# Kernel tuning notes

Measured on AMD Instinct MI355X. Metric: run time of the kernel, lower is better.

Reference implementation:

```python
import jax, jax.numpy as jnp
import numpy as np

NUM_HEADS = 8
KEY_DIM = 256
VALUE_DIM = 256


def setup_inputs() -> dict:
    key = jax.random.key(0)
    kx, km, kq, kk, kv, ko = jax.random.split(key, 6)
    x = jax.random.normal(kx, (8, 32, 32, KEY_DIM), dtype=jnp.float32)
    m = jax.random.normal(km, (8, 32, 32, KEY_DIM), dtype=jnp.float32)
    query_proj = jax.random.normal(kq, (NUM_HEADS, KEY_DIM, KEY_DIM), dtype=jnp.float32)
    key_proj = jax.random.normal(kk, (KEY_DIM, KEY_DIM), dtype=jnp.float32)
    value_proj = jax.random.normal(kv, (KEY_DIM, VALUE_DIM), dtype=jnp.float32)
    output_proj = jax.random.normal(ko, (KEY_DIM, NUM_HEADS, VALUE_DIM), dtype=jnp.float32)
    return {"x": x, "m": m, "query_proj": query_proj, "key_proj": key_proj,
            "value_proj": value_proj, "output_proj": output_proj}


def reference(x, m, query_proj, key_proj, value_proj, output_proj):
    b = x.shape[0]
    d = x.shape[-1]  # == key_dim
    xr = x.reshape(b, -1, d)   # [b, n, d]
    mr = m.reshape(b, -1, d)   # [b, s, d]
    # Per-head query projection; shared (multi-query) key/value projections.
    q = jnp.einsum('bnd,hdk->bnhk', xr, query_proj)            # [b, n, h, k]
    k = jnp.einsum('bsd,dk->bsk', mr, key_proj)                # [b, s, k] shared across heads
    logits = jnp.einsum('bnhk,bsk->bnhs', q, k) / jnp.sqrt(jnp.asarray(d, x.dtype))
    attn = jax.nn.softmax(logits, axis=-1)                      # dropout p=0.0 -> identity
    v = jnp.einsum('bsd,dv->bsv', mr, value_proj)              # [b, s, v] shared across heads
    o = jnp.einsum('bnhs,bsv->bnhv', attn, v)                  # [b, n, h, v]
    out = jnp.einsum('bnhv,dhv->bnd', o, output_proj)          # back to key_dim channels
    return out.reshape(x.shape)
```

## Files before the change

### kernel.cpp

```cpp
#include <hip/hip_runtime.h>
#include <math.h>


typedef short bf16x8 __attribute__((ext_vector_type(8)));
typedef float f32x4  __attribute__((ext_vector_type(4)));

#define MFMA(a, b, c) __builtin_amdgcn_mfma_f32_16x16x32_bf16((a), (b), (c), 0, 0, 0)

typedef __attribute__((address_space(3))) unsigned int lds_u32_t;
typedef __attribute__((address_space(1))) const unsigned int glb_u32_t;

__device__ __forceinline__ unsigned short f32_bf16(float f) {
  unsigned u = __float_as_uint(f);
  u += 0x7FFFu + ((u >> 16) & 1u);
  return (unsigned short)(u >> 16);
}
__device__ __forceinline__ float bf16_f32(unsigned short h) {
  return __uint_as_float(((unsigned)h) << 16);
}

__global__ void k_prep(const float* __restrict__ x, const float* __restrict__ m,
                       const float* __restrict__ op, const float* __restrict__ qp,
                       const float* __restrict__ kp, const float* __restrict__ vp,
                       unsigned short* __restrict__ xh, unsigned short* __restrict__ xl,
                       unsigned short* __restrict__ mh, unsigned short* __restrict__ ml,
                       unsigned short* __restrict__ opb,
                       unsigned short* __restrict__ qph, unsigned short* __restrict__ qpl,
                       unsigned short* __restrict__ kph, unsigned short* __restrict__ kpl,
                       unsigned short* __restrict__ vpt) {
  const int tid = blockIdx.x * blockDim.x + threadIdx.x;
  const int stride = gridDim.x * blockDim.x;
  for (int i = tid; i < 2097152; i += stride) {
    float v = x[i];
    unsigned short h = f32_bf16(v);
    xh[i] = h; xl[i] = f32_bf16(v - bf16_f32(h));
    float w = m[i];
    unsigned short h2 = f32_bf16(w);
    mh[i] = h2; ml[i] = f32_bf16(w - bf16_f32(h2));
  }
  for (int i = tid; i < 524288; i += stride) {
    opb[i] = f32_bf16(op[i]);
    float q = qp[i];
    unsigned short h = f32_bf16(q);
    qph[i] = h; qpl[i] = f32_bf16(q - bf16_f32(h));
  }
  for (int i = tid; i < 65536; i += stride) {
    float k = kp[i];
    unsigned short h = f32_bf16(k);
    kph[i] = h; kpl[i] = f32_bf16(k - bf16_f32(h));
    const int vc = i >> 8, d = i & 255;
    vpt[i] = f32_bf16(vp[d * 256 + vc]);
  }
}

__global__ __launch_bounds__(256) void k_w(
    const unsigned short* __restrict__ qph, const unsigned short* __restrict__ qpl,
    const unsigned short* __restrict__ kph, const unsigned short* __restrict__ kpl,
    unsigned short* __restrict__ wh, unsigned short* __restrict__ wl) {
  const int jt = blockIdx.x & 7;
  const int h  = blockIdx.x >> 3;
  const int wave = threadIdx.x >> 6;
  const int lane = threadIdx.x & 63;
  const int lr = lane & 15, lg = lane >> 4;

  f32x4 acc[2][4];
  const f32x4 z = {0.f, 0.f, 0.f, 0.f};
#pragma unroll
  for (int mi = 0; mi < 2; ++mi)
#pragma unroll
    for (int nt = 0; nt < 4; ++nt) acc[mi][nt] = z;

  for (int ks = 0; ks < 8; ++ks) {
    bf16x8 ah[2], al[2], bh[4], bl[4];
#pragma unroll
    for (int mi = 0; mi < 2; ++mi) {
      const size_t aoff = ((size_t)(jt * 32 + mi * 16 + lr)) * 256 + ks * 32 + lg * 8;
      ah[mi] = *(const bf16x8*)(kph + aoff);
      al[mi] = *(const bf16x8*)(kpl + aoff);
    }
#pragma unroll
    for (int nt = 0; nt < 4; ++nt) {
      const size_t boff = ((size_t)(h * 256 + wave * 64 + nt * 16 + lr)) * 256 + ks * 32 + lg * 8;
      bh[nt] = *(const bf16x8*)(qph + boff);
      bl[nt] = *(const bf16x8*)(qpl + boff);
    }
#pragma unroll
    for (int nt = 0; nt < 4; ++nt)
#pragma unroll
      for (int mi = 0; mi < 2; ++mi) {
        acc[mi][nt] = MFMA(ah[mi], bh[nt], acc[mi][nt]);
        acc[mi][nt] = MFMA(ah[mi], bl[nt], acc[mi][nt]);
        acc[mi][nt] = MFMA(al[mi], bh[nt], acc[mi][nt]);
      }
  }
#pragma unroll
  for (int mi = 0; mi < 2; ++mi)
#pragma unroll
    for (int nt = 0; nt < 4; ++nt)
#pragma unroll
      for (int r = 0; r < 4; ++r) {
        const int j = jt * 32 + mi * 16 + lg * 4 + r;
        const int i = wave * 64 + nt * 16 + lr;
        const float v = acc[mi][nt][r];
        const size_t idx = ((size_t)(h * 256 + j)) * 256 + i;
        const unsigned short hi = f32_bf16(v);
        wh[idx] = hi;
        wl[idx] = f32_bf16(v - bf16_f32(hi));
      }
}

__global__ __launch_bounds__(256) void k_v(
    const unsigned short* __restrict__ vpt, const unsigned short* __restrict__ mh,
    unsigned short* __restrict__ vt) {
  const int sc  = blockIdx.x & 3;
  const int vct = (blockIdx.x >> 2) & 7;
  const int b   = blockIdx.x >> 5;
  const int wave = threadIdx.x >> 6;
  const int lane = threadIdx.x & 63;
  const int lr = lane & 15, lg = lane >> 4;

  f32x4 acc[2][4];
  const f32x4 z = {0.f, 0.f, 0.f, 0.f};
#pragma unroll
  for (int mi = 0; mi < 2; ++mi)
#pragma unroll
    for (int nt = 0; nt < 4; ++nt) acc[mi][nt] = z;

  for (int ks = 0; ks < 8; ++ks) {
    bf16x8 av[2], bv[4];
#pragma unroll
    for (int mi = 0; mi < 2; ++mi)
      av[mi] = *(const bf16x8*)(vpt + ((size_t)(vct * 32 + mi * 16 + lr)) * 256 + ks * 32 + lg * 8);
#pragma unroll
    for (int nt = 0; nt < 4; ++nt)
      bv[nt] = *(const bf16x8*)(mh + ((size_t)(b * 1024 + sc * 256 + wave * 64 + nt * 16 + lr)) * 256 + ks * 32 + lg * 8);
#pragma unroll
    for (int nt = 0; nt < 4; ++nt)
#pragma unroll
      for (int mi = 0; mi < 2; ++mi)
        acc[mi][nt] = MFMA(av[mi], bv[nt], acc[mi][nt]);
  }
#pragma unroll
  for (int mi = 0; mi < 2; ++mi)
#pragma unroll
    for (int nt = 0; nt < 4; ++nt)
#pragma unroll
      for (int r = 0; r < 4; ++r) {
        const int vc = vct * 32 + mi * 16 + lg * 4 + r;
        const int s  = sc * 256 + wave * 64 + nt * 16 + lr;
        vt[((size_t)(b * 256 + vc)) * 1024 + s] = f32_bf16(acc[mi][nt][r]);
      }
}

__global__ __launch_bounds__(256) void k_t(
    const unsigned short* __restrict__ xh, const unsigned short* __restrict__ xl,
    const unsigned short* __restrict__ wh, const unsigned short* __restrict__ wl,
    unsigned short* __restrict__ th, unsigned short* __restrict__ tl) {
  const int wg = blockIdx.x;
  const int mt = wg & 31;
  const int h  = (wg >> 5) & 7;
  const int b  = wg >> 8;
  const int wave = threadIdx.x >> 6;
  const int lane = threadIdx.x & 63;
  const int lr = lane & 15, lg = lane >> 4;

  f32x4 acc[2][4];
  const f32x4 z = {0.f, 0.f, 0.f, 0.f};
#pragma unroll
  for (int mi = 0; mi < 2; ++mi)
#pragma unroll
    for (int nt = 0; nt < 4; ++nt) acc[mi][nt] = z;

  for (int ks = 0; ks < 8; ++ks) {
    bf16x8 ahv[2], alv[2], bh4[4], bl4[4];
#pragma unroll
    for (int mi = 0; mi < 2; ++mi) {
      const size_t aoff = ((size_t)(b * 1024 + mt * 32 + mi * 16 + lr)) * 256 + ks * 32 + lg * 8;
      ahv[mi] = *(const bf16x8*)(xh + aoff);
      alv[mi] = *(const bf16x8*)(xl + aoff);
    }
#pragma unroll
    for (int nt = 0; nt < 4; ++nt) {
      const int dc = wave * 64 + nt * 16 + lr;
      const size_t boff = ((size_t)(h * 256 + dc)) * 256 + ks * 32 + lg * 8;
      bh4[nt] = *(const bf16x8*)(wh + boff);
      bl4[nt] = *(const bf16x8*)(wl + boff);
    }
#pragma unroll
    for (int nt = 0; nt < 4; ++nt)
#pragma unroll
      for (int mi = 0; mi < 2; ++mi) {
        acc[mi][nt] = MFMA(ahv[mi], bh4[nt], acc[mi][nt]);
        acc[mi][nt] = MFMA(ahv[mi], bl4[nt], acc[mi][nt]);
        acc[mi][nt] = MFMA(alv[mi], bh4[nt], acc[mi][nt]);
      }
  }
#pragma unroll
  for (int mi = 0; mi < 2; ++mi)
#pragma unroll
    for (int nt = 0; nt < 4; ++nt)
#pragma unroll
      for (int r = 0; r < 4; ++r) {
        const int row = mt * 32 + mi * 16 + lg * 4 + r;
        const int dc  = wave * 64 + nt * 16 + lr;
        const float v = acc[mi][nt][r];
        const size_t idx = ((size_t)((b * 8 + h) * 1024 + row)) * 256 + dc;
        const unsigned short hi = f32_bf16(v);
        th[idx] = hi;
        tl[idx] = f32_bf16(v - bf16_f32(hi));
      }
}

__global__ __launch_bounds__(512, 2) void k_attn(
    const unsigned short* __restrict__ th, const unsigned short* __restrict__ tl,
    const unsigned short* __restrict__ mh, const unsigned short* __restrict__ ml,
    const unsigned short* __restrict__ vt, unsigned short* __restrict__ ob) {
  __shared__ __align__(16) unsigned short KH[2][8192];
  __shared__ __align__(16) unsigned short KL[2][8192];
  __shared__ __align__(16) unsigned short VB[3][8192];

  const int wg0 = blockIdx.x;
  const int wg = (wg0 & 7) * 64 + (wg0 >> 3);
  const int qt = wg & 7;
  const int h  = (wg >> 3) & 7;
  const int b  = wg >> 6;
  const int wv = threadIdx.x >> 6;
  const int lane = threadIdx.x & 63;
  const int lr = lane & 15, lg = lane >> 4;
  const int start = ((qt << 2) + h) & 31;

  const size_t trow = ((size_t)((b * 8 + h) * 1024 + qt * 128 + wv * 16 + lr)) * 256;
  bf16x8 Th[8], Tl[8];
#pragma unroll
  for (int d = 0; d < 8; ++d) {
    Th[d] = *(const bf16x8*)(th + trow + d * 32 + lg * 8);
    Tl[d] = *(const bf16x8*)(tl + trow + d * 32 + lg * 8);
  }

  const size_t mbase = (size_t)b * 1024 * 256;
  const size_t vbase = (size_t)b * 256 * 1024;

  auto stageK = [&](int lblk, int bi) {
    const int pb = (lblk + start) & 31;
#pragma unroll
    for (int i = 0; i < 2; ++i) {
      const int U = wv * 128 + i * 64 + lane;
      const int s_loc = U >> 5, u_phys = U & 31;
      const int u_log = u_phys ^ (s_loc & 7);
      const size_t soff = mbase + ((size_t)(pb * 32 + s_loc)) * 256 + u_log * 8;
      const int dstb = (wv * 128 + i * 64) * 8;
      __builtin_amdgcn_global_load_lds((glb_u32_t*)(mh + soff), (lds_u32_t*)&KH[bi][dstb], 16, 0, 0);
      __builtin_amdgcn_global_load_lds((glb_u32_t*)(ml + soff), (lds_u32_t*)&KL[bi][dstb], 16, 0, 0);
    }
  };
  auto stageV = [&](int lblk, int vi) {
    const int pb = (lblk + start) & 31;
#pragma unroll
    for (int i = 0; i < 2; ++i) {
      const int U = wv * 128 + i * 64 + lane;
      const int vc = U >> 2, u = U & 3;
      const int u_log = u ^ (vc & 3);
      const size_t soff = vbase + (size_t)vc * 1024 + pb * 32 + u_log * 8;
      const int dstb = (wv * 128 + i * 64) * 8;
      __builtin_amdgcn_global_load_lds((glb_u32_t*)(vt + soff), (lds_u32_t*)&VB[vi][dstb], 16, 0, 0);
    }
  };

  f32x4 Oacc[16];
  const f32x4 z = {0.f, 0.f, 0.f, 0.f};
#pragma unroll
  for (int i = 0; i < 16; ++i) Oacc[i] = z;
  float mrun = -1e30f, lrun = 0.0f;
  const float C16 = 0.0901679993f;

  stageK(0, 0); stageV(0, 0);
  stageK(1, 1); stageV(1, 1);
  asm volatile("s_waitcnt vmcnt(0)" ::: "memory");
  __builtin_amdgcn_s_barrier();

  int pvb = 0;
#pragma unroll 1
  for (int blk = 0; blk < 32; ++blk) {
    const int p = blk & 1;

    f32x4 Sa0 = z, Sb0 = z, Sc0 = z, Sa1 = z, Sb1 = z, Sc1 = z;
#pragma unroll
    for (int d = 0; d < 8; ++d) {
      const int u0 = ((d * 4 + lg) ^ (lr & 7)) * 8;
      const bf16x8 a0h = *(const bf16x8*)&KH[p][lr * 256 + u0];
      const bf16x8 a1h = *(const bf16x8*)&KH[p][(16 + lr) * 256 + u0];
      const bf16x8 a0l = *(const bf16x8*)&KL[p][lr * 256 + u0];
      const bf16x8 a1l = *(const bf16x8*)&KL[p][(16 + lr) * 256 + u0];
      Sa0 = MFMA(a0h, Th[d], Sa0);  Sa1 = MFMA(a1h, Th[d], Sa1);
      Sb0 = MFMA(a0h, Tl[d], Sb0);  Sb1 = MFMA(a1h, Tl[d], Sb1);
      Sc0 = MFMA(a0l, Th[d], Sc0);  Sc1 = MFMA(a1l, Th[d], Sc1);
    }
    const f32x4 S0 = (Sa0 + Sb0) + Sc0;
    const f32x4 S1 = (Sa1 + Sb1) + Sc1;

    float bm = fmaxf(fmaxf(fmaxf(S0[0], S0[1]), fmaxf(S0[2], S0[3])),
                     fmaxf(fmaxf(S1[0], S1[1]), fmaxf(S1[2], S1[3])));
    bm = fmaxf(bm, __shfl_xor(bm, 16));
    bm = fmaxf(bm, __shfl_xor(bm, 32));
    if (!__all(bm - mrun <= 128.0f)) {
      const float mnew = fmaxf(mrun, bm);
      const float sc = exp2f((mrun - mnew) * C16);
      const float s0 = __shfl(sc, lg * 4 + 0);
      const float s1 = __shfl(sc, lg * 4 + 1);
      const float s2 = __shfl(sc, lg * 4 + 2);
      const float s3 = __shfl(sc, lg * 4 + 3);
#pragma unroll
      for (int nt = 0; nt < 16; ++nt) {
        Oacc[nt][0] *= s0; Oacc[nt][1] *= s1; Oacc[nt][2] *= s2; Oacc[nt][3] *= s3;
      }
      lrun *= sc;
      mrun = mnew;
    }
    float p0[4], p1[4];
#pragma unroll
    for (int r = 0; r < 4; ++r) {
      p0[r] = exp2f((S0[r] - mrun) * C16);
      p1[r] = exp2f((S1[r] - mrun) * C16);
    }
    float rs = ((p0[0] + p0[1]) + (p0[2] + p0[3])) +
               ((p1[0] + p1[1]) + (p1[2] + p1[3]));
    rs += __shfl_xor(rs, 16);
    rs += __shfl_xor(rs, 32);
    lrun += rs;

    int D00, D01, D10, D11;
    asm("v_cvt_pk_bf16_f32 %0, %1, %2" : "=v"(D00) : "v"(p0[0]), "v"(p0[1]));
    asm("v_cvt_pk_bf16_f32 %0, %1, %2" : "=v"(D01) : "v"(p0[2]), "v"(p0[3]));
    asm("v_cvt_pk_bf16_f32 %0, %1, %2" : "=v"(D10) : "v"(p1[0]), "v"(p1[1]));
    asm("v_cvt_pk_bf16_f32 %0, %1, %2" : "=v"(D11) : "v"(p1[2]), "v"(p1[3]));
    const bool hi2 = (lg & 2) != 0;
    const bool b1  = (lg & 1) != 0;
    const int own0 = hi2 ? D10 : D00;
    const int own1 = hi2 ? D11 : D01;
    const int ant0 = hi2 ? D00 : D10;
    const int ant1 = hi2 ? D01 : D11;
    const int X0 = __shfl_xor(own0, 16);
    const int X1 = __shfl_xor(own1, 16);
    const int W0 = __shfl_xor(ant0, 32);
    const int W1 = __shfl_xor(ant1, 32);
    const int Y0 = __shfl_xor(W0, 16);
    const int Y1 = __shfl_xor(W1, 16);
    const int F0 = hi2 ? (b1 ? X0 : W0) : (b1 ? Y0 : own0);
    const int F1 = hi2 ? (b1 ? X1 : W1) : (b1 ? Y1 : own1);
    const int G0 = hi2 ? (b1 ? own0 : Y0) : (b1 ? W0 : X0);
    const int G1 = hi2 ? (b1 ? own1 : Y1) : (b1 ? W1 : X1);
    union { int u[4]; bf16x8 v; } pa;
    pa.u[0] = F0; pa.u[1] = F1; pa.u[2] = G0; pa.u[3] = G1;

    asm volatile("s_waitcnt vmcnt(0)" ::: "memory");
    __builtin_amdgcn_s_barrier();

#pragma unroll
    for (int nt = 0; nt < 16; ++nt) {
      const bf16x8 bv = *(const bf16x8*)&VB[pvb][(nt * 16 + lr) * 32 + (lg ^ (lr & 3)) * 8];
      Oacc[nt] = MFMA(pa.v, bv, Oacc[nt]);
    }

    if (blk < 30) {
      stageK(blk + 2, p);
      const int sv = (pvb >= 1) ? pvb - 1 : 2;
      stageV(blk + 2, sv);
    }
    pvb = (pvb == 2) ? 0 : pvb + 1;
  }

  const float inv = 1.0f / lrun;
  const float i0 = __shfl(inv, lg * 4 + 0);
  const float i1 = __shfl(inv, lg * 4 + 1);
  const float i2 = __shfl(inv, lg * 4 + 2);
  const float i3 = __shfl(inv, lg * 4 + 3);
  const int qg = qt * 128 + wv * 16 + lg * 4;
  const size_t obase = ((size_t)(b * 1024 + qg) * 8 + h) * 256 + lr;
#pragma unroll
  for (int nt = 0; nt < 16; ++nt) {
    ob[obase + 0 * 2048 + nt * 16] = f32_bf16(Oacc[nt][0] * i0);
    ob[obase + 1 * 2048 + nt * 16] = f32_bf16(Oacc[nt][1] * i1);
    ob[obase + 2 * 2048 + nt * 16] = f32_bf16(Oacc[nt][2] * i2);
    ob[obase + 3 * 2048 + nt * 16] = f32_bf16(Oacc[nt][3] * i3);
  }
}

__global__ __launch_bounds__(256) void k_out(
    const unsigned short* __restrict__ ob, const unsigned short* __restrict__ opb,
    float* __restrict__ out) {
  const int wg = blockIdx.x;
  const int wave = threadIdx.x >> 6;
  const int lane = threadIdx.x & 63;
  const int lr = lane & 15, lg = lane >> 4;

  f32x4 acc[2][4];
  const f32x4 z = {0.f, 0.f, 0.f, 0.f};
#pragma unroll
  for (int mi = 0; mi < 2; ++mi)
#pragma unroll
    for (int nt = 0; nt < 4; ++nt) acc[mi][nt] = z;

  for (int ks = 0; ks < 64; ++ks) {
    bf16x8 av[2], bv[4];
#pragma unroll
    for (int mi = 0; mi < 2; ++mi) {
      const size_t aoff = ((size_t)(wg * 32 + mi * 16 + lr)) * 2048 + ks * 32 + lg * 8;
      av[mi] = *(const bf16x8*)(ob + aoff);
    }
#pragma unroll
    for (int nt = 0; nt < 4; ++nt) {
      const int dc = wave * 64 + nt * 16 + lr;
      bv[nt] = *(const bf16x8*)(opb + ((size_t)dc) * 2048 + ks * 32 + lg * 8);
    }
#pragma unroll
    for (int nt = 0; nt < 4; ++nt)
#pragma unroll
      for (int mi = 0; mi < 2; ++mi)
        acc[mi][nt] = MFMA(av[mi], bv[nt], acc[mi][nt]);
  }
#pragma unroll
  for (int mi = 0; mi < 2; ++mi)
#pragma unroll
    for (int nt = 0; nt < 4; ++nt)
#pragma unroll
      for (int r = 0; r < 4; ++r) {
        const int row = wg * 32 + mi * 16 + lg * 4 + r;
        const int dc  = wave * 64 + nt * 16 + lr;
        out[(size_t)row * 256 + dc] = acc[mi][nt][r];
      }
}

extern "C" void kernel_launch(void* const* d_in, const int* in_sizes, int n_in,
                              void* d_out, int out_size, void* d_ws, size_t ws_size,
                              hipStream_t stream) {
  const float* x  = (const float*)d_in[0];
  const float* m  = (const float*)d_in[1];
  const float* qp = (const float*)d_in[2];
  const float* kp = (const float*)d_in[3];
  const float* vp = (const float*)d_in[4];
  const float* op = (const float*)d_in[5];
  float* out = (float*)d_out;

  unsigned short* xh  = (unsigned short*)d_ws;
  unsigned short* xl  = xh  + 2097152;
  unsigned short* mh  = xl  + 2097152;
  unsigned short* ml  = mh  + 2097152;
  unsigned short* wh  = ml  + 2097152;
  unsigned short* wl  = wh  + 524288;
  unsigned short* opb = wl  + 524288;
  unsigned short* vt  = opb + 524288;
  unsigned short* th  = vt  + 2097152;
  unsigned short* tl  = th  + 16777216;
  unsigned short* ob  = tl  + 16777216;
  unsigned short* qph = ob  + 16777216;
  unsigned short* qpl = qph + 524288;
  unsigned short* kph = qpl + 524288;
  unsigned short* kpl = kph + 65536;
  unsigned short* vpt = kpl + 65536;

  k_prep<<<2048, 256, 0, stream>>>(x, m, op, qp, kp, vp, xh, xl, mh, ml, opb,
                                   qph, qpl, kph, kpl, vpt);
  k_w   <<<64,   256, 0, stream>>>(qph, qpl, kph, kpl, wh, wl);
  k_v   <<<256,  256, 0, stream>>>(vpt, mh, vt);
  k_t   <<<2048, 256, 0, stream>>>(xh, xl, wh, wl, th, tl);
  k_attn<<<512,  512, 0, stream>>>(th, tl, mh, ml, vt, ob);
  k_out <<<256,  256, 0, stream>>>(ob, opb, out);
}
```

Before: 344.9 us.

## Shrink attention key tiles to 16, use fp16 PV MFMA, raise occupancy

The attention kernel now processes 16 keys per block instead of 32, halving LDS buffers so four workgroups can be resident per CU. V is stored as fp16 and the PV product uses a 16x16x16 f16 MFMA, which removes the cross-lane shuffle repacking of P. The 1/16 logit scale moves into the T producer so softmax uses plain log2e, and the rescale threshold becomes 8. The trade is twice as many loop iterations, each with its own barrier, and smaller MFMA work per barrier, plus fp16 range/precision risk on V.

```diff
diff --git a/kernel.cpp b/kernel.cpp
--- a/kernel.cpp
+++ b/kernel.cpp
@@ -3,9 +3,11 @@
 
 
 typedef short bf16x8 __attribute__((ext_vector_type(8)));
+typedef __fp16 f16x4 __attribute__((ext_vector_type(4)));
 typedef float f32x4  __attribute__((ext_vector_type(4)));
 
-#define MFMA(a, b, c) __builtin_amdgcn_mfma_f32_16x16x32_bf16((a), (b), (c), 0, 0, 0)
+#define MFMA(a, b, c)   __builtin_amdgcn_mfma_f32_16x16x32_bf16((a), (b), (c), 0, 0, 0)
+#define MFMA16(a, b, c) __builtin_amdgcn_mfma_f32_16x16x16f16((a), (b), (c), 0, 0, 0)
 
 typedef __attribute__((address_space(3))) unsigned int lds_u32_t;
 typedef __attribute__((address_space(1))) const unsigned int glb_u32_t;
@@ -111,7 +113,7 @@
 
 __global__ __launch_bounds__(256) void k_v(
     const unsigned short* __restrict__ vpt, const unsigned short* __restrict__ mh,
-    unsigned short* __restrict__ vt) {
+    __fp16* __restrict__ vt) {
   const int sc  = blockIdx.x & 3;
   const int vct = (blockIdx.x >> 2) & 7;
   const int b   = blockIdx.x >> 5;
@@ -148,7 +150,7 @@
       for (int r = 0; r < 4; ++r) {
         const int vc = vct * 32 + mi * 16 + lg * 4 + r;
         const int s  = sc * 256 + wave * 64 + nt * 16 + lr;
-        vt[((size_t)(b * 256 + vc)) * 1024 + s] = f32_bf16(acc[mi][nt][r]);
+        vt[((size_t)(b * 256 + vc)) * 1024 + s] = (__fp16)acc[mi][nt][r];
       }
 }
 
@@ -203,7 +205,7 @@
       for (int r = 0; r < 4; ++r) {
         const int row = mt * 32 + mi * 16 + lg * 4 + r;
         const int dc  = wave * 64 + nt * 16 + lr;
-        const float v = acc[mi][nt][r];
+        const float v = acc[mi][nt][r] * 0.0625f;
         const size_t idx = ((size_t)((b * 8 + h) * 1024 + row)) * 256 + dc;
         const unsigned short hi = f32_bf16(v);
         th[idx] = hi;
@@ -211,13 +213,13 @@
       }
 }
 
-__global__ __launch_bounds__(512, 2) void k_attn(
+__global__ __launch_bounds__(512, 4) void k_attn(
     const unsigned short* __restrict__ th, const unsigned short* __restrict__ tl,
     const unsigned short* __restrict__ mh, const unsigned short* __restrict__ ml,
-    const unsigned short* __restrict__ vt, unsigned short* __restrict__ ob) {
-  __shared__ __align__(16) unsigned short KH[2][8192];
-  __shared__ __align__(16) unsigned short KL[2][8192];
-  __shared__ __align__(16) unsigned short VB[3][8192];
+    const __fp16* __restrict__ vt, unsigned short* __restrict__ ob) {
+  __shared__ __align__(16) unsigned short KH[2][4096];
+  __shared__ __align__(16) unsigned short KL[2][4096];
+  __shared__ __align__(16) __fp16         VB[2][4096];
 
   const int wg0 = blockIdx.x;
   const int wg = (wg0 & 7) * 64 + (wg0 >> 3);
@@ -227,7 +229,7 @@
   const int wv = threadIdx.x >> 6;
   const int lane = threadIdx.x & 63;
   const int lr = lane & 15, lg = lane >> 4;
-  const int start = ((qt << 2) + h) & 31;
+  const int start = ((qt << 3) + h) & 63;
 
   const size_t trow = ((size_t)((b * 8 + h) * 1024 + qt * 128 + wv * 16 + lr)) * 256;
   bf16x8 Th[8], Tl[8];
@@ -241,29 +243,21 @@
   const size_t vbase = (size_t)b * 256 * 1024;
 
   auto stageK = [&](int lblk, int bi) {
-    const int pb = (lblk + start) & 31;
-#pragma unroll
-    for (int i = 0; i < 2; ++i) {
-      const int U = wv * 128 + i * 64 + lane;
-      const int s_loc = U >> 5, u_phys = U & 31;
-      const int u_log = u_phys ^ (s_loc & 7);
-      const size_t soff = mbase + ((size_t)(pb * 32 + s_loc)) * 256 + u_log * 8;
-      const int dstb = (wv * 128 + i * 64) * 8;
-      __builtin_amdgcn_global_load_lds((glb_u32_t*)(mh + soff), (lds_u32_t*)&KH[bi][dstb], 16, 0, 0);
-      __builtin_amdgcn_global_load_lds((glb_u32_t*)(ml + soff), (lds_u32_t*)&KL[bi][dstb], 16, 0, 0);
-    }
+    const int U = wv * 64 + lane;
+    const int s_loc = U >> 5, u_phys = U & 31;
+    const int u_log = u_phys ^ (s_loc & 7);
+    const int pb = (lblk + start) & 63;
+    const size_t soff = mbase + ((size_t)(pb * 16 + s_loc)) * 256 + u_log * 8;
+    const int dsts = U * 8;
+    __builtin_amdgcn_global_load_lds((glb_u32_t*)(mh + soff), (lds_u32_t*)&KH[bi][dsts], 16, 0, 0);
+    __builtin_amdgcn_global_load_lds((glb_u32_t*)(ml + soff), (lds_u32_t*)&KL[bi][dsts], 16, 0, 0);
   };
-  auto stageV = [&](int lblk, int vi) {
-    const int pb = (lblk + start) & 31;
-#pragma unroll
-    for (int i = 0; i < 2; ++i) {
-      const int U = wv * 128 + i * 64 + lane;
-      const int vc = U >> 2, u = U & 3;
-      const int u_log = u ^ (vc & 3);
-      const size_t soff = vbase + (size_t)vc * 1024 + pb * 32 + u_log * 8;
-      const int dstb = (wv * 128 + i * 64) * 8;
-      __builtin_amdgcn_global_load_lds((glb_u32_t*)(vt + soff), (lds_u32_t*)&VB[vi][dstb], 16, 0, 0);
-    }
+  auto stageV = [&](int lblk, int bi) {
+    const int U = wv * 64 + lane;
+    const int vc = U >> 1, u = U & 1;
+    const int pb = (lblk + start) & 63;
+    const size_t soff = vbase + (size_t)vc * 1024 + pb * 16 + u * 8;
+    __builtin_amdgcn_global_load_lds((glb_u32_t*)(vt + soff), (lds_u32_t*)&VB[bi][U * 8], 16, 0, 0);
   };
 
   f32x4 Oacc[16];
@@ -271,40 +265,35 @@
 #pragma unroll
   for (int i = 0; i < 16; ++i) Oacc[i] = z;
   float mrun = -1e30f, lrun = 0.0f;
-  const float C16 = 0.0901679993f;
+  const float LOG2E = 1.44269504f;
 
   stageK(0, 0); stageV(0, 0);
   stageK(1, 1); stageV(1, 1);
-  asm volatile("s_waitcnt vmcnt(0)" ::: "memory");
+  asm volatile("s_waitcnt vmcnt(3)" ::: "memory");
   __builtin_amdgcn_s_barrier();
 
-  int pvb = 0;
 #pragma unroll 1
-  for (int blk = 0; blk < 32; ++blk) {
+  for (int blk = 0; blk < 64; ++blk) {
     const int p = blk & 1;
 
-    f32x4 Sa0 = z, Sb0 = z, Sc0 = z, Sa1 = z, Sb1 = z, Sc1 = z;
+    f32x4 Sa = z, Sb = z, Sc = z;
 #pragma unroll
     for (int d = 0; d < 8; ++d) {
       const int u0 = ((d * 4 + lg) ^ (lr & 7)) * 8;
-      const bf16x8 a0h = *(const bf16x8*)&KH[p][lr * 256 + u0];
-      const bf16x8 a1h = *(const bf16x8*)&KH[p][(16 + lr) * 256 + u0];
-      const bf16x8 a0l = *(const bf16x8*)&KL[p][lr * 256 + u0];
-      const bf16x8 a1l = *(const bf16x8*)&KL[p][(16 + lr) * 256 + u0];
-      Sa0 = MFMA(a0h, Th[d], Sa0);  Sa1 = MFMA(a1h, Th[d], Sa1);
-      Sb0 = MFMA(a0h, Tl[d], Sb0);  Sb1 = MFMA(a1h, Tl[d], Sb1);
-      Sc0 = MFMA(a0l, Th[d], Sc0);  Sc1 = MFMA(a1l, Th[d], Sc1);
-    }
-    const f32x4 S0 = (Sa0 + Sb0) + Sc0;
-    const f32x4 S1 = (Sa1 + Sb1) + Sc1;
-
-    float bm = fmaxf(fmaxf(fmaxf(S0[0], S0[1]), fmaxf(S0[2], S0[3])),
-                     fmaxf(fmaxf(S1[0], S1[1]), fmaxf(S1[2], S1[3])));
+      const bf16x8 a_h = *(const bf16x8*)&KH[p][lr * 256 + u0];
+      const bf16x8 a_l = *(const bf16x8*)&KL[p][lr * 256 + u0];
+      Sa = MFMA(a_h, Th[d], Sa);
+      Sb = MFMA(a_h, Tl[d], Sb);
+      Sc = MFMA(a_l, Th[d], Sc);
+    }
+    const f32x4 S = (Sa + Sb) + Sc;
+
+    float bm = fmaxf(fmaxf(S[0], S[1]), fmaxf(S[2], S[3]));
     bm = fmaxf(bm, __shfl_xor(bm, 16));
     bm = fmaxf(bm, __shfl_xor(bm, 32));
-    if (!__all(bm - mrun <= 128.0f)) {
+    if (!__all(bm - mrun <= 8.0f)) {
       const float mnew = fmaxf(mrun, bm);
-      const float sc = exp2f((mrun - mnew) * C16);
+      const float sc = exp2f((mrun - mnew) * LOG2E);
       const float s0 = __shfl(sc, lg * 4 + 0);
       const float s1 = __shfl(sc, lg * 4 + 1);
       const float s2 = __shfl(sc, lg * 4 + 2);
@@ -316,57 +305,30 @@
       lrun *= sc;
       mrun = mnew;
     }
-    float p0[4], p1[4];
-#pragma unroll
-    for (int r = 0; r < 4; ++r) {
-      p0[r] = exp2f((S0[r] - mrun) * C16);
-      p1[r] = exp2f((S1[r] - mrun) * C16);
-    }
-    float rs = ((p0[0] + p0[1]) + (p0[2] + p0[3])) +
-               ((p1[0] + p1[1]) + (p1[2] + p1[3]));
+    float pr[4];
+#pragma unroll
+    for (int r = 0; r < 4; ++r) pr[r] = exp2f((S[r] - mrun) * LOG2E);
+    float rs = (pr[0] + pr[1]) + (pr[2] + pr[3]);
     rs += __shfl_xor(rs, 16);
     rs += __shfl_xor(rs, 32);
     lrun += rs;
 
-    int D00, D01, D10, D11;
-    asm("v_cvt_pk_bf16_f32 %0, %1, %2" : "=v"(D00) : "v"(p0[0]), "v"(p0[1]));
-    asm("v_cvt_pk_bf16_f32 %0, %1, %2" : "=v"(D01) : "v"(p0[2]), "v"(p0[3]));
-    asm("v_cvt_pk_bf16_f32 %0, %1, %2" : "=v"(D10) : "v"(p1[0]), "v"(p1[1]));
-    asm("v_cvt_pk_bf16_f32 %0, %1, %2" : "=v"(D11) : "v"(p1[2]), "v"(p1[3]));
-    const bool hi2 = (lg & 2) != 0;
-    const bool b1  = (lg & 1) != 0;
-    const int own0 = hi2 ? D10 : D00;
-    const int own1 = hi2 ? D11 : D01;
-    const int ant0 = hi2 ? D00 : D10;
-    const int ant1 = hi2 ? D01 : D11;
-    const int X0 = __shfl_xor(own0, 16);
-    const int X1 = __shfl_xor(own1, 16);
-    const int W0 = __shfl_xor(ant0, 32);
-    const int W1 = __shfl_xor(ant1, 32);
-    const int Y0 = __shfl_xor(W0, 16);
-    const int Y1 = __shfl_xor(W1, 16);
-    const int F0 = hi2 ? (b1 ? X0 : W0) : (b1 ? Y0 : own0);
-    const int F1 = hi2 ? (b1 ? X1 : W1) : (b1 ? Y1 : own1);
-    const int G0 = hi2 ? (b1 ? own0 : Y0) : (b1 ? W0 : X0);
-    const int G1 = hi2 ? (b1 ? own1 : Y1) : (b1 ? W1 : X1);
-    union { int u[4]; bf16x8 v; } pa;
-    pa.u[0] = F0; pa.u[1] = F1; pa.u[2] = G0; pa.u[3] = G1;
-
-    asm volatile("s_waitcnt vmcnt(0)" ::: "memory");
-    __builtin_amdgcn_s_barrier();
+    const auto c01 = __builtin_amdgcn_cvt_pkrtz(pr[0], pr[1]);
+    const auto c23 = __builtin_amdgcn_cvt_pkrtz(pr[2], pr[3]);
+    f16x4 pa;
+    pa[0] = c01[0]; pa[1] = c01[1]; pa[2] = c23[0]; pa[3] = c23[1];
 
 #pragma unroll
     for (int nt = 0; nt < 16; ++nt) {
-      const bf16x8 bv = *(const bf16x8*)&VB[pvb][(nt * 16 + lr) * 32 + (lg ^ (lr & 3)) * 8];
-      Oacc[nt] = MFMA(pa.v, bv, Oacc[nt]);
-    }
-
-    if (blk < 30) {
-      stageK(blk + 2, p);
-      const int sv = (pvb >= 1) ? pvb - 1 : 2;
-      stageV(blk + 2, sv);
-    }
-    pvb = (pvb == 2) ? 0 : pvb + 1;
+      const f16x4 bv = *(const f16x4*)&VB[p][(nt * 16 + lr) * 16 + lg * 4];
+      Oacc[nt] = MFMA16(pa, bv, Oacc[nt]);
+    }
+
+    if (blk < 63) {
+      asm volatile("s_waitcnt vmcnt(0)" ::: "memory");
+      __builtin_amdgcn_s_barrier();
+      if (blk < 62) { stageK(blk + 2, p); stageV(blk + 2, p); }
+    }
   }
 
   const float inv = 1.0f / lrun;
@@ -448,8 +410,8 @@
   unsigned short* wh  = ml  + 2097152;
   unsigned short* wl  = wh  + 524288;
   unsigned short* opb = wl  + 524288;
-  unsigned short* vt  = opb + 524288;
-  unsigned short* th  = vt  + 2097152;
+  __fp16*         vt  = (__fp16*)(opb + 524288);
+  unsigned short* th  = (unsigned short*)(vt + 2097152);
   unsigned short* tl  = th  + 16777216;
   unsigned short* ob  = tl  + 16777216;
   unsigned short* qph = ob  + 16777216;
```

Measured after the change: 923.3 us. 168% more time.
